# Optimization experiments

Measured on AMD Instinct MI355X. Metric: run time of the kernel, lower is better.

The kernel has to match this reference:

```python
import jax, jax.numpy as jnp
import numpy as np

B, S, D_MODEL, H, OUT = 32, 64, 256, 256, 10
N_POS = 64  # n_max_seq + 1


def _coordinate_map():
    i = jnp.arange(N_POS, dtype=jnp.float32)
    r = jnp.sqrt(jnp.float32(N_POS))
    c0 = (i / r - 2.0) / 2.0
    c1 = (jnp.mod(i, r) - 2.0) / 2.0
    coord = jnp.stack([c0, c1], axis=-1)            # [N_POS, 2]
    return jnp.broadcast_to(coord[None], (B, N_POS, 2))


def setup_inputs() -> dict:
    key = jax.random.key(0)
    ks = jax.random.split(key, 13)
    d_in = (D_MODEL + 2) * 3
    w = lambda k, i, o: jax.random.normal(k, (i, o), jnp.float32) * 0.02
    b = lambda k, o: jax.random.normal(k, (o,), jnp.float32) * 0.02
    return {
        'sentences': jax.random.normal(ks[0], (B, S, D_MODEL), jnp.float32),
        'coord': _coordinate_map(),
        'g_w1': w(ks[1], d_in, H), 'g_b1': b(ks[2], H),
        'g_w2': w(ks[3], H, H),    'g_b2': b(ks[4], H),
        'g_w3': w(ks[5], H, H),    'g_b3': b(ks[6], H),
        'f_w1': w(ks[7], H, H),    'f_b1': b(ks[8], H),
        'f_w2': w(ks[9], H, H),    'f_b2': b(ks[10], H),
        'f_w3': w(ks[11], H, OUT), 'f_b3': b(ks[12], OUT),
    }


def reference(sentences, coord, g_w1, g_b1, g_w2, g_b2, g_w3, g_b3,
              f_w1, f_b1, f_w2, f_b2, f_w3, f_b3):
    b, s, d = sentences.shape
    x = jnp.concatenate([sentences, coord[:b, :s, :]], axis=-1)   # [B,S,D+2]
    oi = jnp.broadcast_to(x[:, None, :, :], (b, s, s, d + 2))     # object_i[b,i,j]=x[b,j]
    oj = jnp.broadcast_to(x[:, :, None, :], (b, s, s, d + 2))     # object_j[b,i,j]=x[b,i]
    pairs = jnp.concatenate([oi, oj, oi * oj], axis=-1)           # [B,S,S,3*(D+2)]
    h = jax.nn.relu(jnp.einsum('bijk,kh->bijh', pairs, g_w1) + g_b1)
    h = jax.nn.relu(h @ g_w2 + g_b2)
    h = jax.nn.relu(h @ g_w3 + g_b3)
    rel = h.reshape(b, s * s, -1).sum(axis=1)                     # [B,H]
    y = jax.nn.relu(rel @ f_w1 + f_b1)
    y = jax.nn.relu(y @ f_w2 + f_b2)                              # Dropout: eval mode (identity)
    return y @ f_w3 + f_b3                                        # [B,OUT]
```

## Files before the change

### kernel.cpp

```cpp
#include <hip/hip_runtime.h>
#include <hip/hip_bf16.h>


typedef __attribute__((ext_vector_type(4))) float f32x4;
typedef __attribute__((ext_vector_type(16))) float f32x16;
typedef __attribute__((ext_vector_type(8))) short frag8;
typedef __attribute__((ext_vector_type(4))) unsigned u32x4;

__device__ __forceinline__ float bf2f(short s) {
  return __uint_as_float(((unsigned)(unsigned short)s) << 16);
}
__device__ __forceinline__ short f2bf(float f) {
  unsigned u = __float_as_uint(f);
  return (short)((u + 0x7fffu + ((u >> 16) & 1u)) >> 16);
}

__device__ __forceinline__ unsigned pk_bf16(float lo, float hi) {
#if __has_builtin(__builtin_amdgcn_cvt_pk_bf16_f32)
  return __builtin_bit_cast(unsigned, __builtin_amdgcn_cvt_pk_bf16_f32(lo, hi));
#else
  unsigned ul = __float_as_uint(lo), uh = __float_as_uint(hi);
  ul = (ul + 0x7fffu + ((ul >> 16) & 1u)) >> 16;
  uh = (uh + 0x7fffu + ((uh >> 16) & 1u)) & 0xffff0000u;
  return ul | uh;
#endif
}

__device__ __forceinline__ unsigned pk_mul_bf16(unsigned a, unsigned b) {
  float al = __uint_as_float(a << 16);
  float ah = __uint_as_float(a & 0xffff0000u);
  float bl = __uint_as_float(b << 16);
  float bh = __uint_as_float(b & 0xffff0000u);
  return pk_bf16(al * bl, ah * bh);
}

__device__ __forceinline__ frag8 pk_mul4(u32x4 a, u32x4 b) {
  u32x4 r;
#pragma unroll
  for (int t = 0; t < 4; t++) r[t] = pk_mul_bf16(a[t], b[t]);
  return __builtin_bit_cast(frag8, r);
}

#define KX 288

__global__ __launch_bounds__(256)
void prep(const float* __restrict__ sent, const float* __restrict__ coord,
          const float* __restrict__ g_w1, const float* __restrict__ g_w2,
          const float* __restrict__ g_w3,
          short* __restrict__ xb, short* __restrict__ Wab, short* __restrict__ Wc,
          short* __restrict__ W2t, short* __restrict__ W3t, float* __restrict__ rel) {
  __shared__ short tile[64 * 66];
  const int blk = blockIdx.x, t = threadIdx.x;

  if (blk < 288) {
    long idx0 = ((long)blk * 256 + t) * 8;
#pragma unroll
    for (int e = 0; e < 8; e++) {
      long idx = idx0 + e;
      int row = (int)(idx / KX), k = (int)(idx - (long)row * KX);
      float v = 0.f;
      if (k < 256)      v = sent[(size_t)row * 256 + k];
      else if (k < 258) v = coord[row * 2 + (k - 256)];
      xb[idx] = f2bf(v);
    }
    return;
  }

  const int nc = t & 63, r4 = t >> 6;
  if (blk < 328) {
    int tt = blk - 288, kt = tt >> 3, nt = tt & 7;
    int k0 = kt * 64, n0 = nt * 64;
    for (int p = 0; p < 16; p++) {
      int kl = p * 4 + r4, k = k0 + kl, n = n0 + nc;
      float v = 0.f;
      if (k < 258) {
        int row = (n < 256) ? k : 258 + k;
        int col = (n < 256) ? n : n - 256;
        v = g_w1[(size_t)row * 256 + col];
      }
      tile[kl * 66 + nc] = f2bf(v);
    }
    __syncthreads();
    for (int p = 0; p < 16; p++) {
      int nl = p * 4 + r4;
      if (k0 + nc < KX) Wab[(size_t)(n0 + nl) * KX + k0 + nc] = tile[nc * 66 + nl];
    }
    return;
  }
  if (blk < 348) {
    int tt = blk - 328, kt = tt >> 2, nt = tt & 3;
    int k0 = kt * 64, n0 = nt * 64;
    for (int p = 0; p < 16; p++) {
      int kl = p * 4 + r4, k = k0 + kl;
      float v = (k < 258) ? g_w1[(size_t)(516 + k) * 256 + n0 + nc] : 0.f;
      tile[kl * 66 + nc] = f2bf(v);
    }
    __syncthreads();
    for (int p = 0; p < 16; p++) {
      int nl = p * 4 + r4;
      if (k0 + nc < KX) Wc[(size_t)(n0 + nl) * KX + k0 + nc] = tile[nc * 66 + nl];
    }
    return;
  }
  if (blk < 380) {
    int tt = blk - 348;
    const float* W = (tt < 16) ? g_w2 : g_w3;
    short* Wt = (tt < 16) ? W2t : W3t;
    tt &= 15;
    int k0 = (tt >> 2) * 64, n0 = (tt & 3) * 64;
    for (int p = 0; p < 16; p++) {
      int kl = p * 4 + r4;
      tile[kl * 66 + nc] = f2bf(W[(size_t)(k0 + kl) * 256 + n0 + nc]);
    }
    __syncthreads();
    for (int p = 0; p < 16; p++) {
      int nl = p * 4 + r4;
      Wt[(size_t)(n0 + nl) * 256 + k0 + nc] = tile[nc * 66 + nl];
    }
    return;
  }
  {
    int bb = blk - 380;
    ((f32x4*)rel)[bb * 256 + t] = (f32x4){0.f, 0.f, 0.f, 0.f};
  }
}


__global__ __launch_bounds__(64)
void uv_gemm(const short* __restrict__ xb, const short* __restrict__ Wab,
             const float* __restrict__ g_b1, float* __restrict__ uv) {
  const int m0 = blockIdx.x * 64;
  const int n0 = blockIdx.y * 64;
  const int lane = threadIdx.x;
  const int q = lane >> 4, l16 = lane & 15;

  f32x4 acc[4][4];
#pragma unroll
  for (int mt = 0; mt < 4; mt++)
#pragma unroll
    for (int nt = 0; nt < 4; nt++) acc[mt][nt] = (f32x4){0.f, 0.f, 0.f, 0.f};

  for (int k0 = 0; k0 < KX; k0 += 32) {
    frag8 a[4], bb[4];
#pragma unroll
    for (int mt = 0; mt < 4; mt++)
      a[mt] = *(const frag8*)(xb + (size_t)(m0 + mt * 16 + l16) * KX + k0 + q * 8);
#pragma unroll
    for (int nt = 0; nt < 4; nt++)
      bb[nt] = *(const frag8*)(Wab + (size_t)(n0 + nt * 16 + l16) * KX + k0 + q * 8);
#pragma unroll
    for (int mt = 0; mt < 4; mt++)
#pragma unroll
      for (int nt = 0; nt < 4; nt++)
        acc[mt][nt] = __builtin_amdgcn_mfma_f32_16x16x32_bf16(a[mt], bb[nt], acc[mt][nt], 0, 0, 0);
  }
#pragma unroll
  for (int nt = 0; nt < 4; nt++) {
    int col = n0 + nt * 16 + l16;
    float bias = (col >= 256) ? g_b1[col - 256] : 0.f;
#pragma unroll
    for (int mt = 0; mt < 4; mt++) {
      int m = m0 + mt * 16 + q * 4;
#pragma unroll
      for (int r = 0; r < 4; r++)
        uv[(size_t)(m + r) * 512 + col] = acc[mt][nt][r] + bias;
    }
  }
}


#define LDS_SHORTS 32768

__global__ __launch_bounds__(256, 2)
void relnet_main(const short* __restrict__ xb, const short* __restrict__ Wc,
                 const short* __restrict__ W2t, const short* __restrict__ W3t,
                 const float* __restrict__ uv, const float* __restrict__ g_b2,
                 const float* __restrict__ g_b3, float* __restrict__ rel) {
  __shared__ short lds[LDS_SHORTS];

  const int tid = threadIdx.x;
  const int bi = blockIdx.x;
  const int b = bi >> 5, ip = bi & 31;
  const int i0 = ip * 2;
  const int lane = tid & 63, wave = tid >> 6;
  const int l32 = lane & 31, half = lane >> 5;
  const int n0 = wave * 64;
  const int rowbase = b * 64;

  f32x16 acc[4][2];
#pragma unroll
  for (int mt = 0; mt < 4; mt++)
#pragma unroll
    for (int nt = 0; nt < 2; nt++)
#pragma unroll
      for (int r = 0; r < 16; r++) acc[mt][nt][r] = 0.f;

  {
    const short* xjl = xb + (size_t)(rowbase + l32) * KX;
    const short* xjh = xb + (size_t)(rowbase + 32 + l32) * KX;
    const short* xi0p = xb + (size_t)(rowbase + i0) * KX;
    const short* xi1p = xb + (size_t)(rowbase + i0 + 1) * KX;
    const short* wc0 = Wc + (size_t)(n0 + l32) * KX;
    const short* wc1 = Wc + (size_t)(n0 + 32 + l32) * KX;

    u32x4 jl0, jh0, ia0, ib0, jl1, jh1, ia1, ib1;
    frag8 b0[2], b1[2];
    {
      int k = half * 8;
      jl0 = *(const u32x4*)(xjl + k);
      jh0 = *(const u32x4*)(xjh + k);
      ia0 = *(const u32x4*)(xi0p + k);
      ib0 = *(const u32x4*)(xi1p + k);
      b0[0] = *(const frag8*)(wc0 + k);
      b0[1] = *(const frag8*)(wc1 + k);
    }
#pragma unroll
    for (int ks = 0; ks < 18; ks++) {
      if (ks < 17) {
        int k = (ks + 1) * 16 + half * 8;
        jl1 = *(const u32x4*)(xjl + k);
        jh1 = *(const u32x4*)(xjh + k);
        ia1 = *(const u32x4*)(xi0p + k);
        ib1 = *(const u32x4*)(xi1p + k);
        b1[0] = *(const frag8*)(wc0 + k);
        b1[1] = *(const frag8*)(wc1 + k);
      }
      frag8 a[4];
      a[0] = pk_mul4(jl0, ia0);
      a[1] = pk_mul4(jh0, ia0);
      a[2] = pk_mul4(jl0, ib0);
      a[3] = pk_mul4(jh0, ib0);
#pragma unroll
      for (int mt = 0; mt < 4; mt++)
#pragma unroll
        for (int nt = 0; nt < 2; nt++)
          acc[mt][nt] = __builtin_amdgcn_mfma_f32_32x32x16_bf16(a[mt], b0[nt], acc[mt][nt], 0, 0, 0);
      jl0 = jl1; jh0 = jh1; ia0 = ia1; ib0 = ib1;
      b0[0] = b1[0]; b0[1] = b1[1];
    }
  }

  {
    const float* ub = uv + (size_t)rowbase * 512;
    const float* v0p = uv + (size_t)(rowbase + i0) * 512 + 256;
    const float* v1p = uv + (size_t)(rowbase + i0 + 1) * 512 + 256;
#pragma unroll
    for (int nt = 0; nt < 2; nt++) {
      int col = n0 + nt * 32 + l32;
      int cb = (n0 + nt * 32) >> 3;
      float vv0 = v0p[col], vv1 = v1p[col];
#pragma unroll
      for (int mt = 0; mt < 4; mt++) {
        float vv = (mt < 2) ? vv0 : vv1;
#pragma unroll
        for (int r = 0; r < 16; r += 2) {
          int rb0 = (r & 3) + 8 * (r >> 2) + 4 * half;
          int jm0 = (mt & 1) * 32 + rb0;
          float x0 = fmaxf(acc[mt][nt][r]     + ub[(size_t)jm0 * 512 + col] + vv, 0.f);
          float x1 = fmaxf(acc[mt][nt][r + 1] + ub[(size_t)(jm0 + 1) * 512 + col] + vv, 0.f);
          unsigned pk = pk_bf16(x0, x1);
          int m0r = mt * 32 + rb0;
          int sw0 = (r & 3) + 4 * half;
          lds[m0r * 256 + (((cb + (l32 >> 3)) ^ sw0) << 3) + (l32 & 7)] = (short)(pk & 0xffffu);
          lds[(m0r + 1) * 256 + (((cb + (l32 >> 3)) ^ (sw0 + 1)) << 3) + (l32 & 7)] = (short)(pk >> 16);
        }
#pragma unroll
        for (int r = 0; r < 16; r++) acc[mt][nt][r] = 0.f;
      }
    }
  }
  __syncthreads();

  {
    const int swr = l32 & 7;
    frag8 a0[4], b0[2], a1[4], b1[2];
#pragma unroll
    for (int mt = 0; mt < 4; mt++)
      a0[mt] = *(const frag8*)(&lds[(mt * 32 + l32) * 256 + ((half ^ swr) << 3)]);
#pragma unroll
    for (int nt = 0; nt < 2; nt++)
      b0[nt] = *(const frag8*)(W2t + (size_t)(n0 + nt * 32 + l32) * 256 + half * 8);
#pragma unroll
    for (int ks = 0; ks < 16; ks++) {
      if (ks < 15) {
        int c1 = ((2 * (ks + 1) + half) ^ swr) << 3;
        int k1 = (ks + 1) * 16 + half * 8;
#pragma unroll
        for (int mt = 0; mt < 4; mt++)
          a1[mt] = *(const frag8*)(&lds[(mt * 32 + l32) * 256 + c1]);
#pragma unroll
        for (int nt = 0; nt < 2; nt++)
          b1[nt] = *(const frag8*)(W2t + (size_t)(n0 + nt * 32 + l32) * 256 + k1);
      }
#pragma unroll
      for (int mt = 0; mt < 4; mt++)
#pragma unroll
        for (int nt = 0; nt < 2; nt++)
          acc[mt][nt] = __builtin_amdgcn_mfma_f32_32x32x16_bf16(a0[mt], b0[nt], acc[mt][nt], 0, 0, 0);
#pragma unroll
      for (int mt = 0; mt < 4; mt++) a0[mt] = a1[mt];
#pragma unroll
      for (int nt = 0; nt < 2; nt++) b0[nt] = b1[nt];
    }
  }
  __syncthreads();
#pragma unroll
  for (int nt = 0; nt < 2; nt++) {
    int col = n0 + nt * 32 + l32;
    int cb = (n0 + nt * 32) >> 3;
    float b2 = g_b2[col];
#pragma unroll
    for (int mt = 0; mt < 4; mt++) {
#pragma unroll
      for (int r = 0; r < 16; r += 2) {
        int rb0 = (r & 3) + 8 * (r >> 2) + 4 * half;
        float x0 = fmaxf(acc[mt][nt][r] + b2, 0.f);
        float x1 = fmaxf(acc[mt][nt][r + 1] + b2, 0.f);
        unsigned pk = pk_bf16(x0, x1);
        int m0r = mt * 32 + rb0;
        int sw0 = (r & 3) + 4 * half;
        lds[m0r * 256 + (((cb + (l32 >> 3)) ^ sw0) << 3) + (l32 & 7)] = (short)(pk & 0xffffu);
        lds[(m0r + 1) * 256 + (((cb + (l32 >> 3)) ^ (sw0 + 1)) << 3) + (l32 & 7)] = (short)(pk >> 16);
      }
#pragma unroll
      for (int r = 0; r < 16; r++) acc[mt][nt][r] = 0.f;
    }
  }
  __syncthreads();

  {
    const int swr = l32 & 7;
    frag8 a0[4], b0[2], a1[4], b1[2];
#pragma unroll
    for (int mt = 0; mt < 4; mt++)
      a0[mt] = *(const frag8*)(&lds[(mt * 32 + l32) * 256 + ((half ^ swr) << 3)]);
#pragma unroll
    for (int nt = 0; nt < 2; nt++)
      b0[nt] = *(const frag8*)(W3t + (size_t)(n0 + nt * 32 + l32) * 256 + half * 8);
#pragma unroll
    for (int ks = 0; ks < 16; ks++) {
      if (ks < 15) {
        int c1 = ((2 * (ks + 1) + half) ^ swr) << 3;
        int k1 = (ks + 1) * 16 + half * 8;
#pragma unroll
        for (int mt = 0; mt < 4; mt++)
          a1[mt] = *(const frag8*)(&lds[(mt * 32 + l32) * 256 + c1]);
#pragma unroll
        for (int nt = 0; nt < 2; nt++)
          b1[nt] = *(const frag8*)(W3t + (size_t)(n0 + nt * 32 + l32) * 256 + k1);
      }
#pragma unroll
      for (int mt = 0; mt < 4; mt++)
#pragma unroll
        for (int nt = 0; nt < 2; nt++)
          acc[mt][nt] = __builtin_amdgcn_mfma_f32_32x32x16_bf16(a0[mt], b0[nt], acc[mt][nt], 0, 0, 0);
#pragma unroll
      for (int mt = 0; mt < 4; mt++) a0[mt] = a1[mt];
#pragma unroll
      for (int nt = 0; nt < 2; nt++) b0[nt] = b1[nt];
    }
  }
#pragma unroll
  for (int nt = 0; nt < 2; nt++) {
    int col = n0 + nt * 32 + l32;
    float b3 = g_b3[col];
    float s = 0.f;
#pragma unroll
    for (int mt = 0; mt < 4; mt++)
#pragma unroll
      for (int r = 0; r < 16; r++)
        s += fmaxf(acc[mt][nt][r] + b3, 0.f);
    s += __shfl_xor(s, 32, 64);
    if (half == 0) atomicAdd(&rel[b * 256 + col], s);
  }
}

__global__ __launch_bounds__(256)
void fnet(const float* __restrict__ rel, const float* __restrict__ f_w1,
          const float* __restrict__ f_b1, const float* __restrict__ f_w2,
          const float* __restrict__ f_b2, const float* __restrict__ f_w3,
          const float* __restrict__ f_b3, float* __restrict__ out) {
  int b = blockIdx.x, t = threadIdx.x;
  __shared__ float y0[256], y1[256], y2[256];
  y0[t] = rel[b * 256 + t];
  __syncthreads();
  float s = f_b1[t];
#pragma unroll 8
  for (int k = 0; k < 256; k++) s += y0[k] * f_w1[k * 256 + t];
  y1[t] = fmaxf(s, 0.f);
  __syncthreads();
  s = f_b2[t];
#pragma unroll 8
  for (int k = 0; k < 256; k++) s += y1[k] * f_w2[k * 256 + t];
  y2[t] = fmaxf(s, 0.f);
  __syncthreads();
  if (t < 10) {
    float s2 = f_b3[t];
#pragma unroll 8
    for (int k = 0; k < 256; k++) s2 += y2[k] * f_w3[k * 10 + t];
    out[b * 10 + t] = s2;
  }
}

extern "C" void kernel_launch(void* const* d_in, const int* in_sizes, int n_in,
                              void* d_out, int out_size, void* d_ws, size_t ws_size,
                              hipStream_t stream) {
  const float* sent  = (const float*)d_in[0];
  const float* coord = (const float*)d_in[1];
  const float* g_w1  = (const float*)d_in[2];
  const float* g_b1  = (const float*)d_in[3];
  const float* g_w2  = (const float*)d_in[4];
  const float* g_b2  = (const float*)d_in[5];
  const float* g_w3  = (const float*)d_in[6];
  const float* g_b3  = (const float*)d_in[7];
  const float* f_w1  = (const float*)d_in[8];
  const float* f_b1  = (const float*)d_in[9];
  const float* f_w2  = (const float*)d_in[10];
  const float* f_b2  = (const float*)d_in[11];
  const float* f_w3  = (const float*)d_in[12];
  const float* f_b3  = (const float*)d_in[13];
  float* out = (float*)d_out;

  char* ws = (char*)d_ws;
  size_t off = 0;
  auto alloc = [&](size_t bytes) {
    char* p = ws + off;
    off += (bytes + 255) & ~(size_t)255;
    return p;
  };
  short* xb  = (short*)alloc((size_t)2048 * KX * 2);
  short* Wab = (short*)alloc((size_t)512 * KX * 2);
  short* Wc  = (short*)alloc((size_t)256 * KX * 2);
  short* W2t = (short*)alloc((size_t)256 * 256 * 2);
  short* W3t = (short*)alloc((size_t)256 * 256 * 2);
  float* uv  = (float*)alloc((size_t)2048 * 512 * 4);
  float* rel = (float*)alloc((size_t)32 * 256 * 4);

  prep<<<388, 256, 0, stream>>>(sent, coord, g_w1, g_w2, g_w3, xb, Wab, Wc, W2t, W3t, rel);
  uv_gemm<<<dim3(32, 8), 64, 0, stream>>>(xb, Wab, g_b1, uv);
  relnet_main<<<1024, 256, 0, stream>>>(xb, Wc, W2t, W3t, uv, g_b2, g_b3, rel);
  fnet<<<32, 256, 0, stream>>>(rel, f_w1, f_b1, f_w2, f_b2, f_w3, f_b3, out);
}
```

Baseline: 195.2 us.

## Stage pair products in LDS, transpose u buffer, double-buffer weight fragments

```diff
diff --git a/kernel.cpp b/kernel.cpp
--- a/kernel.cpp
+++ b/kernel.cpp
@@ -42,6 +42,7 @@
 }
 
 #define KX 288
+#define KS 272
 
 __global__ __launch_bounds__(256)
 void prep(const float* __restrict__ sent, const float* __restrict__ coord,
@@ -128,7 +129,8 @@
 
 __global__ __launch_bounds__(64)
 void uv_gemm(const short* __restrict__ xb, const short* __restrict__ Wab,
-             const float* __restrict__ g_b1, float* __restrict__ uv) {
+             const float* __restrict__ g_b1, float* __restrict__ uT,
+             float* __restrict__ vbuf) {
   const int m0 = blockIdx.x * 64;
   const int n0 = blockIdx.y * 64;
   const int lane = threadIdx.x;
@@ -154,28 +156,40 @@
       for (int nt = 0; nt < 4; nt++)
         acc[mt][nt] = __builtin_amdgcn_mfma_f32_16x16x32_bf16(a[mt], bb[nt], acc[mt][nt], 0, 0, 0);
   }
-#pragma unroll
-  for (int nt = 0; nt < 4; nt++) {
-    int col = n0 + nt * 16 + l16;
-    float bias = (col >= 256) ? g_b1[col - 256] : 0.f;
-#pragma unroll
-    for (int mt = 0; mt < 4; mt++) {
-      int m = m0 + mt * 16 + q * 4;
-#pragma unroll
-      for (int r = 0; r < 4; r++)
-        uv[(size_t)(m + r) * 512 + col] = acc[mt][nt][r] + bias;
-    }
-  }
-}
-
-
-#define LDS_SHORTS 32768
+  if (n0 < 256) {
+#pragma unroll
+    for (int nt = 0; nt < 4; nt++) {
+      int col = n0 + nt * 16 + l16;
+#pragma unroll
+      for (int mt = 0; mt < 4; mt++)
+        *(f32x4*)(uT + ((size_t)blockIdx.x * 256 + col) * 64 + mt * 16 + q * 4) = acc[mt][nt];
+    }
+  } else {
+#pragma unroll
+    for (int nt = 0; nt < 4; nt++) {
+      int c = n0 - 256 + nt * 16 + l16;
+      float bias = g_b1[c];
+#pragma unroll
+      for (int mt = 0; mt < 4; mt++) {
+        int m = m0 + mt * 16 + q * 4;
+#pragma unroll
+        for (int r = 0; r < 4; r++)
+          vbuf[(size_t)(m + r) * 256 + c] = acc[mt][nt][r] + bias;
+      }
+    }
+  }
+}
+
+
+#define ASH 280
+#define LDS_SHORTS (128 * ASH)
 
 __global__ __launch_bounds__(256, 2)
 void relnet_main(const short* __restrict__ xb, const short* __restrict__ Wc,
                  const short* __restrict__ W2t, const short* __restrict__ W3t,
-                 const float* __restrict__ uv, const float* __restrict__ g_b2,
-                 const float* __restrict__ g_b3, float* __restrict__ rel) {
+                 const float* __restrict__ uT, const float* __restrict__ vbuf,
+                 const float* __restrict__ g_b2, const float* __restrict__ g_b3,
+                 float* __restrict__ rel) {
   __shared__ short lds[LDS_SHORTS];
 
   const int tid = threadIdx.x;
@@ -186,6 +200,7 @@
   const int l32 = lane & 31, half = lane >> 5;
   const int n0 = wave * 64;
   const int rowbase = b * 64;
+  const int swr = l32 & 7;
 
   f32x16 acc[4][2];
 #pragma unroll
@@ -195,60 +210,52 @@
 #pragma unroll
       for (int r = 0; r < 16; r++) acc[mt][nt][r] = 0.f;
 
+#pragma unroll
+  for (int it = 0; it < 17; it++) {
+    int idx = tid + it * 256;
+    int j = idx / 34, c = idx - j * 34;
+    int k = c * 8;
+    u32x4 aj = *(const u32x4*)(xb + (size_t)(rowbase + (j & 63)) * KX + k);
+    u32x4 ai = *(const u32x4*)(xb + (size_t)(rowbase + i0 + (j >> 6)) * KX + k);
+    *(frag8*)(&lds[j * ASH + k]) = pk_mul4(aj, ai);
+  }
+
+  const short* wc0 = Wc + (size_t)(n0 + l32) * KX + half * 8;
+  const short* wc1 = Wc + (size_t)(n0 + 32 + l32) * KX + half * 8;
+  frag8 bp[2][2];
+  bp[0][0] = *(const frag8*)(wc0);
+  bp[0][1] = *(const frag8*)(wc1);
+  bp[1][0] = *(const frag8*)(wc0 + 16);
+  bp[1][1] = *(const frag8*)(wc1 + 16);
+  __syncthreads();
+
+#pragma unroll
+  for (int ks = 0; ks < 17; ks++) {
+    frag8 bc0 = bp[ks & 1][0], bc1 = bp[ks & 1][1];
+    if (ks + 2 < 17) {
+      bp[ks & 1][0] = *(const frag8*)(wc0 + (ks + 2) * 16);
+      bp[ks & 1][1] = *(const frag8*)(wc1 + (ks + 2) * 16);
+    }
+    frag8 a[4];
+#pragma unroll
+    for (int mt = 0; mt < 4; mt++)
+      a[mt] = *(const frag8*)(&lds[(mt * 32 + l32) * ASH + ks * 16 + half * 8]);
+#pragma unroll
+    for (int mt = 0; mt < 4; mt++) {
+      acc[mt][0] = __builtin_amdgcn_mfma_f32_32x32x16_bf16(a[mt], bc0, acc[mt][0], 0, 0, 0);
+      acc[mt][1] = __builtin_amdgcn_mfma_f32_32x32x16_bf16(a[mt], bc1, acc[mt][1], 0, 0, 0);
+    }
+  }
+  __syncthreads();
+
   {
-    const short* xjl = xb + (size_t)(rowbase + l32) * KX;
-    const short* xjh = xb + (size_t)(rowbase + 32 + l32) * KX;
-    const short* xi0p = xb + (size_t)(rowbase + i0) * KX;
-    const short* xi1p = xb + (size_t)(rowbase + i0 + 1) * KX;
-    const short* wc0 = Wc + (size_t)(n0 + l32) * KX;
-    const short* wc1 = Wc + (size_t)(n0 + 32 + l32) * KX;
-
-    u32x4 jl0, jh0, ia0, ib0, jl1, jh1, ia1, ib1;
-    frag8 b0[2], b1[2];
-    {
-      int k = half * 8;
-      jl0 = *(const u32x4*)(xjl + k);
-      jh0 = *(const u32x4*)(xjh + k);
-      ia0 = *(const u32x4*)(xi0p + k);
-      ib0 = *(const u32x4*)(xi1p + k);
-      b0[0] = *(const frag8*)(wc0 + k);
-      b0[1] = *(const frag8*)(wc1 + k);
-    }
-#pragma unroll
-    for (int ks = 0; ks < 18; ks++) {
-      if (ks < 17) {
-        int k = (ks + 1) * 16 + half * 8;
-        jl1 = *(const u32x4*)(xjl + k);
-        jh1 = *(const u32x4*)(xjh + k);
-        ia1 = *(const u32x4*)(xi0p + k);
-        ib1 = *(const u32x4*)(xi1p + k);
-        b1[0] = *(const frag8*)(wc0 + k);
-        b1[1] = *(const frag8*)(wc1 + k);
-      }
-      frag8 a[4];
-      a[0] = pk_mul4(jl0, ia0);
-      a[1] = pk_mul4(jh0, ia0);
-      a[2] = pk_mul4(jl0, ib0);
-      a[3] = pk_mul4(jh0, ib0);
-#pragma unroll
-      for (int mt = 0; mt < 4; mt++)
-#pragma unroll
-        for (int nt = 0; nt < 2; nt++)
-          acc[mt][nt] = __builtin_amdgcn_mfma_f32_32x32x16_bf16(a[mt], b0[nt], acc[mt][nt], 0, 0, 0);
-      jl0 = jl1; jh0 = jh1; ia0 = ia1; ib0 = ib1;
-      b0[0] = b1[0]; b0[1] = b1[1];
-    }
-  }
-
-  {
-    const float* ub = uv + (size_t)rowbase * 512;
-    const float* v0p = uv + (size_t)(rowbase + i0) * 512 + 256;
-    const float* v1p = uv + (size_t)(rowbase + i0 + 1) * 512 + 256;
 #pragma unroll
     for (int nt = 0; nt < 2; nt++) {
       int col = n0 + nt * 32 + l32;
       int cb = (n0 + nt * 32) >> 3;
-      float vv0 = v0p[col], vv1 = v1p[col];
+      const float* ubp = uT + ((size_t)b * 256 + col) * 64;
+      float vv0 = vbuf[(size_t)(rowbase + i0) * 256 + col];
+      float vv1 = vbuf[(size_t)(rowbase + i0 + 1) * 256 + col];
 #pragma unroll
       for (int mt = 0; mt < 4; mt++) {
         float vv = (mt < 2) ? vv0 : vv1;
@@ -256,8 +263,9 @@
         for (int r = 0; r < 16; r += 2) {
           int rb0 = (r & 3) + 8 * (r >> 2) + 4 * half;
           int jm0 = (mt & 1) * 32 + rb0;
-          float x0 = fmaxf(acc[mt][nt][r]     + ub[(size_t)jm0 * 512 + col] + vv, 0.f);
-          float x1 = fmaxf(acc[mt][nt][r + 1] + ub[(size_t)(jm0 + 1) * 512 + col] + vv, 0.f);
+          float2 uu = *(const float2*)(ubp + jm0);
+          float x0 = fmaxf(acc[mt][nt][r]     + uu.x + vv, 0.f);
+          float x1 = fmaxf(acc[mt][nt][r + 1] + uu.y + vv, 0.f);
           unsigned pk = pk_bf16(x0, x1);
           int m0r = mt * 32 + rb0;
           int sw0 = (r & 3) + 4 * half;
@@ -269,41 +277,33 @@
       }
     }
   }
-  __syncthreads();
-
-  {
-    const int swr = l32 & 7;
-    frag8 a0[4], b0[2], a1[4], b1[2];
-#pragma unroll
-    for (int mt = 0; mt < 4; mt++)
-      a0[mt] = *(const frag8*)(&lds[(mt * 32 + l32) * 256 + ((half ^ swr) << 3)]);
-#pragma unroll
-    for (int nt = 0; nt < 2; nt++)
-      b0[nt] = *(const frag8*)(W2t + (size_t)(n0 + nt * 32 + l32) * 256 + half * 8);
-#pragma unroll
-    for (int ks = 0; ks < 16; ks++) {
-      if (ks < 15) {
-        int c1 = ((2 * (ks + 1) + half) ^ swr) << 3;
-        int k1 = (ks + 1) * 16 + half * 8;
-#pragma unroll
-        for (int mt = 0; mt < 4; mt++)
-          a1[mt] = *(const frag8*)(&lds[(mt * 32 + l32) * 256 + c1]);
-#pragma unroll
-        for (int nt = 0; nt < 2; nt++)
-          b1[nt] = *(const frag8*)(W2t + (size_t)(n0 + nt * 32 + l32) * 256 + k1);
-      }
-#pragma unroll
-      for (int mt = 0; mt < 4; mt++)
-#pragma unroll
-        for (int nt = 0; nt < 2; nt++)
-          acc[mt][nt] = __builtin_amdgcn_mfma_f32_32x32x16_bf16(a0[mt], b0[nt], acc[mt][nt], 0, 0, 0);
-#pragma unroll
-      for (int mt = 0; mt < 4; mt++) a0[mt] = a1[mt];
-#pragma unroll
-      for (int nt = 0; nt < 2; nt++) b0[nt] = b1[nt];
-    }
-  }
-  __syncthreads();
+  const short* w20 = W2t + (size_t)(n0 + l32) * 256 + half * 8;
+  const short* w21 = W2t + (size_t)(n0 + 32 + l32) * 256 + half * 8;
+  bp[0][0] = *(const frag8*)(w20);
+  bp[0][1] = *(const frag8*)(w21);
+  bp[1][0] = *(const frag8*)(w20 + 16);
+  bp[1][1] = *(const frag8*)(w21 + 16);
+  __syncthreads();
+
+#pragma unroll
+  for (int ks = 0; ks < 16; ks++) {
+    frag8 bc0 = bp[ks & 1][0], bc1 = bp[ks & 1][1];
+    if (ks + 2 < 16) {
+      bp[ks & 1][0] = *(const frag8*)(w20 + (ks + 2) * 16);
+      bp[ks & 1][1] = *(const frag8*)(w21 + (ks + 2) * 16);
+    }
+    frag8 a[4];
+#pragma unroll
+    for (int mt = 0; mt < 4; mt++)
+      a[mt] = *(const frag8*)(&lds[(mt * 32 + l32) * 256 + (((2 * ks + half) ^ swr) << 3)]);
+#pragma unroll
+    for (int mt = 0; mt < 4; mt++) {
+      acc[mt][0] = __builtin_amdgcn_mfma_f32_32x32x16_bf16(a[mt], bc0, acc[mt][0], 0, 0, 0);
+      acc[mt][1] = __builtin_amdgcn_mfma_f32_32x32x16_bf16(a[mt], bc1, acc[mt][1], 0, 0, 0);
+    }
+  }
+  __syncthreads();
+
 #pragma unroll
   for (int nt = 0; nt < 2; nt++) {
     int col = n0 + nt * 32 + l32;
@@ -326,38 +326,29 @@
       for (int r = 0; r < 16; r++) acc[mt][nt][r] = 0.f;
     }
   }
-  __syncthreads();
-
-  {
-    const int swr = l32 & 7;
-    frag8 a0[4], b0[2], a1[4], b1[2];
-#pragma unroll
-    for (int mt = 0; mt < 4; mt++)
-      a0[mt] = *(const frag8*)(&lds[(mt * 32 + l32) * 256 + ((half ^ swr) << 3)]);
-#pragma unroll
-    for (int nt = 0; nt < 2; nt++)
-      b0[nt] = *(const frag8*)(W3t + (size_t)(n0 + nt * 32 + l32) * 256 + half * 8);
-#pragma unroll
-    for (int ks = 0; ks < 16; ks++) {
-      if (ks < 15) {
-        int c1 = ((2 * (ks + 1) + half) ^ swr) << 3;
-        int k1 = (ks + 1) * 16 + half * 8;
-#pragma unroll
-        for (int mt = 0; mt < 4; mt++)
-          a1[mt] = *(const frag8*)(&lds[(mt * 32 + l32) * 256 + c1]);
-#pragma unroll
-        for (int nt = 0; nt < 2; nt++)
-          b1[nt] = *(const frag8*)(W3t + (size_t)(n0 + nt * 32 + l32) * 256 + k1);
-      }
-#pragma unroll
-      for (int mt = 0; mt < 4; mt++)
-#pragma unroll
-        for (int nt = 0; nt < 2; nt++)
-          acc[mt][nt] = __builtin_amdgcn_mfma_f32_32x32x16_bf16(a0[mt], b0[nt], acc[mt][nt], 0, 0, 0);
-#pragma unroll
-      for (int mt = 0; mt < 4; mt++) a0[mt] = a1[mt];
-#pragma unroll
-      for (int nt = 0; nt < 2; nt++) b0[nt] = b1[nt];
+  const short* w30 = W3t + (size_t)(n0 + l32) * 256 + half * 8;
+  const short* w31 = W3t + (size_t)(n0 + 32 + l32) * 256 + half * 8;
+  bp[0][0] = *(const frag8*)(w30);
+  bp[0][1] = *(const frag8*)(w31);
+  bp[1][0] = *(const frag8*)(w30 + 16);
+  bp[1][1] = *(const frag8*)(w31 + 16);
+  __syncthreads();
+
+#pragma unroll
+  for (int ks = 0; ks < 16; ks++) {
+    frag8 bc0 = bp[ks & 1][0], bc1 = bp[ks & 1][1];
+    if (ks + 2 < 16) {
+      bp[ks & 1][0] = *(const frag8*)(w30 + (ks + 2) * 16);
+      bp[ks & 1][1] = *(const frag8*)(w31 + (ks + 2) * 16);
+    }
+    frag8 a[4];
+#pragma unroll
+    for (int mt = 0; mt < 4; mt++)
+      a[mt] = *(const frag8*)(&lds[(mt * 32 + l32) * 256 + (((2 * ks + half) ^ swr) << 3)]);
+#pragma unroll
+    for (int mt = 0; mt < 4; mt++) {
+      acc[mt][0] = __builtin_amdgcn_mfma_f32_32x32x16_bf16(a[mt], bc0, acc[mt][0], 0, 0, 0);
+      acc[mt][1] = __builtin_amdgcn_mfma_f32_32x32x16_bf16(a[mt], bc1, acc[mt][1], 0, 0, 0);
     }
   }
 #pragma unroll
@@ -428,16 +419,17 @@
     off += (bytes + 255) & ~(size_t)255;
     return p;
   };
-  short* xb  = (short*)alloc((size_t)2048 * KX * 2);
-  short* Wab = (short*)alloc((size_t)512 * KX * 2);
-  short* Wc  = (short*)alloc((size_t)256 * KX * 2);
-  short* W2t = (short*)alloc((size_t)256 * 256 * 2);
-  short* W3t = (short*)alloc((size_t)256 * 256 * 2);
-  float* uv  = (float*)alloc((size_t)2048 * 512 * 4);
-  float* rel = (float*)alloc((size_t)32 * 256 * 4);
+  short* xb   = (short*)alloc((size_t)2048 * KX * 2);
+  short* Wab  = (short*)alloc((size_t)512 * KX * 2);
+  short* Wc   = (short*)alloc((size_t)256 * KX * 2);
+  short* W2t  = (short*)alloc((size_t)256 * 256 * 2);
+  short* W3t  = (short*)alloc((size_t)256 * 256 * 2);
+  float* uT   = (float*)alloc((size_t)32 * 256 * 64 * 4);
+  float* vbuf = (float*)alloc((size_t)2048 * 256 * 4);
+  float* rel  = (float*)alloc((size_t)32 * 256 * 4);
 
   prep<<<388, 256, 0, stream>>>(sent, coord, g_w1, g_w2, g_w3, xb, Wab, Wc, W2t, W3t, rel);
-  uv_gemm<<<dim3(32, 8), 64, 0, stream>>>(xb, Wab, g_b1, uv);
-  relnet_main<<<1024, 256, 0, stream>>>(xb, Wc, W2t, W3t, uv, g_b2, g_b3, rel);
+  uv_gemm<<<dim3(32, 8), 64, 0, stream>>>(xb, Wab, g_b1, uT, vbuf);
+  relnet_main<<<1024, 256, 0, stream>>>(xb, Wc, W2t, W3t, uT, vbuf, g_b2, g_b3, rel);
   fnet<<<32, 256, 0, stream>>>(rel, f_w1, f_b1, f_w2, f_b2, f_w3, f_b3, out);
 }
```

Measured after the change: 217.5 us. 1.11x slower.

## Stage elementwise-product A tile in LDS once instead of per-wave recompute

Applied to the files above, without the earlier changes.

```diff
diff --git a/kernel.cpp b/kernel.cpp
--- a/kernel.cpp
+++ b/kernel.cpp
@@ -169,7 +169,9 @@
 }
 
 
-#define LDS_SHORTS 32768
+#define ASH 152
+#define A2OFF (128 * ASH)
+#define LDS_SHORTS (2 * 128 * ASH)
 
 __global__ __launch_bounds__(256, 2)
 void relnet_main(const short* __restrict__ xb, const short* __restrict__ Wc,
@@ -186,6 +188,7 @@
   const int l32 = lane & 31, half = lane >> 5;
   const int n0 = wave * 64;
   const int rowbase = b * 64;
+  const int swr = l32 & 7;
 
   f32x16 acc[4][2];
 #pragma unroll
@@ -195,50 +198,90 @@
 #pragma unroll
       for (int r = 0; r < 16; r++) acc[mt][nt][r] = 0.f;
 
-  {
-    const short* xjl = xb + (size_t)(rowbase + l32) * KX;
-    const short* xjh = xb + (size_t)(rowbase + 32 + l32) * KX;
-    const short* xi0p = xb + (size_t)(rowbase + i0) * KX;
-    const short* xi1p = xb + (size_t)(rowbase + i0 + 1) * KX;
-    const short* wc0 = Wc + (size_t)(n0 + l32) * KX;
-    const short* wc1 = Wc + (size_t)(n0 + 32 + l32) * KX;
-
-    u32x4 jl0, jh0, ia0, ib0, jl1, jh1, ia1, ib1;
-    frag8 b0[2], b1[2];
-    {
-      int k = half * 8;
-      jl0 = *(const u32x4*)(xjl + k);
-      jh0 = *(const u32x4*)(xjh + k);
-      ia0 = *(const u32x4*)(xi0p + k);
-      ib0 = *(const u32x4*)(xi1p + k);
-      b0[0] = *(const frag8*)(wc0 + k);
-      b0[1] = *(const frag8*)(wc1 + k);
-    }
-#pragma unroll
-    for (int ks = 0; ks < 18; ks++) {
-      if (ks < 17) {
-        int k = (ks + 1) * 16 + half * 8;
-        jl1 = *(const u32x4*)(xjl + k);
-        jh1 = *(const u32x4*)(xjh + k);
-        ia1 = *(const u32x4*)(xi0p + k);
-        ib1 = *(const u32x4*)(xi1p + k);
-        b1[0] = *(const frag8*)(wc0 + k);
-        b1[1] = *(const frag8*)(wc1 + k);
-      }
-      frag8 a[4];
-      a[0] = pk_mul4(jl0, ia0);
-      a[1] = pk_mul4(jh0, ia0);
-      a[2] = pk_mul4(jl0, ib0);
-      a[3] = pk_mul4(jh0, ib0);
+#pragma unroll
+  for (int it = 0; it < 9; it++) {
+    int idx = tid + it * 256;
+    int j = idx / 18, c = idx - j * 18;
+    int k = c * 8;
+    u32x4 aj = *(const u32x4*)(xb + (size_t)(rowbase + (j & 63)) * KX + k);
+    u32x4 ai = *(const u32x4*)(xb + (size_t)(rowbase + i0 + (j >> 6)) * KX + k);
+    *(frag8*)(&lds[j * ASH + k]) = pk_mul4(aj, ai);
+  }
+  __syncthreads();
+
+  {
+    frag8 a0[4], b0[2], a1[4], b1[2];
+#pragma unroll
+    for (int mt = 0; mt < 4; mt++)
+      a0[mt] = *(const frag8*)(&lds[(mt * 32 + l32) * ASH + half * 8]);
+#pragma unroll
+    for (int nt = 0; nt < 2; nt++)
+      b0[nt] = *(const frag8*)(Wc + (size_t)(n0 + nt * 32 + l32) * KX + half * 8);
+#pragma unroll
+    for (int ks = 0; ks < 9; ks++) {
+      if (ks < 8) {
+        int k1 = (ks + 1) * 16 + half * 8;
+#pragma unroll
+        for (int mt = 0; mt < 4; mt++)
+          a1[mt] = *(const frag8*)(&lds[(mt * 32 + l32) * ASH + k1]);
+#pragma unroll
+        for (int nt = 0; nt < 2; nt++)
+          b1[nt] = *(const frag8*)(Wc + (size_t)(n0 + nt * 32 + l32) * KX + k1);
+      }
 #pragma unroll
       for (int mt = 0; mt < 4; mt++)
 #pragma unroll
         for (int nt = 0; nt < 2; nt++)
-          acc[mt][nt] = __builtin_amdgcn_mfma_f32_32x32x16_bf16(a[mt], b0[nt], acc[mt][nt], 0, 0, 0);
-      jl0 = jl1; jh0 = jh1; ia0 = ia1; ib0 = ib1;
-      b0[0] = b1[0]; b0[1] = b1[1];
-    }
-  }
+          acc[mt][nt] = __builtin_amdgcn_mfma_f32_32x32x16_bf16(a0[mt], b0[nt], acc[mt][nt], 0, 0, 0);
+#pragma unroll
+      for (int mt = 0; mt < 4; mt++) a0[mt] = a1[mt];
+#pragma unroll
+      for (int nt = 0; nt < 2; nt++) b0[nt] = b1[nt];
+    }
+  }
+
+#pragma unroll
+  for (int it = 0; it < 8; it++) {
+    int idx = tid + it * 256;
+    int j = idx >> 4, c = idx & 15;
+    int k = 144 + c * 8;
+    u32x4 aj = *(const u32x4*)(xb + (size_t)(rowbase + (j & 63)) * KX + k);
+    u32x4 ai = *(const u32x4*)(xb + (size_t)(rowbase + i0 + (j >> 6)) * KX + k);
+    *(frag8*)(&lds[A2OFF + j * ASH + c * 8]) = pk_mul4(aj, ai);
+  }
+  __syncthreads();
+
+  {
+    frag8 a0[4], b0[2], a1[4], b1[2];
+#pragma unroll
+    for (int mt = 0; mt < 4; mt++)
+      a0[mt] = *(const frag8*)(&lds[A2OFF + (mt * 32 + l32) * ASH + half * 8]);
+#pragma unroll
+    for (int nt = 0; nt < 2; nt++)
+      b0[nt] = *(const frag8*)(Wc + (size_t)(n0 + nt * 32 + l32) * KX + 144 + half * 8);
+#pragma unroll
+    for (int ks = 0; ks < 8; ks++) {
+      if (ks < 7) {
+        int k1 = (ks + 1) * 16 + half * 8;
+#pragma unroll
+        for (int mt = 0; mt < 4; mt++)
+          a1[mt] = *(const frag8*)(&lds[A2OFF + (mt * 32 + l32) * ASH + k1]);
+#pragma unroll
+        for (int nt = 0; nt < 2; nt++)
+          b1[nt] = *(const frag8*)(Wc + (size_t)(n0 + nt * 32 + l32) * KX + 144 + k1);
+      }
+#pragma unroll
+      for (int mt = 0; mt < 4; mt++)
+#pragma unroll
+        for (int nt = 0; nt < 2; nt++)
+          acc[mt][nt] = __builtin_amdgcn_mfma_f32_32x32x16_bf16(a0[mt], b0[nt], acc[mt][nt], 0, 0, 0);
+#pragma unroll
+      for (int mt = 0; mt < 4; mt++) a0[mt] = a1[mt];
+#pragma unroll
+      for (int nt = 0; nt < 2; nt++) b0[nt] = b1[nt];
+    }
+  }
+  __syncthreads();
 
   {
     const float* ub = uv + (size_t)rowbase * 512;
@@ -272,7 +315,6 @@
   __syncthreads();
 
   {
-    const int swr = l32 & 7;
     frag8 a0[4], b0[2], a1[4], b1[2];
 #pragma unroll
     for (int mt = 0; mt < 4; mt++)
@@ -304,6 +346,7 @@
     }
   }
   __syncthreads();
+
 #pragma unroll
   for (int nt = 0; nt < 2; nt++) {
     int col = n0 + nt * 32 + l32;
@@ -329,7 +372,6 @@
   __syncthreads();
 
   {
-    const int swr = l32 & 7;
     frag8 a0[4], b0[2], a1[4], b1[2];
 #pragma unroll
     for (int mt = 0; mt < 4; mt++)
```

Result: faster. 183.2 us (-6.2%).

## Use 8 waves per block and stage pairwise product tiles in LDS

Applied to the files above, without the earlier changes.

```diff
diff --git a/kernel.cpp b/kernel.cpp
--- a/kernel.cpp
+++ b/kernel.cpp
@@ -169,9 +169,11 @@
 }
 
 
-#define LDS_SHORTS 32768
-
-__global__ __launch_bounds__(256, 2)
+#define ASH 152
+#define A2OFF (128 * ASH)
+#define LDS_SHORTS (2 * 128 * ASH)
+
+__global__ __launch_bounds__(512, 4)
 void relnet_main(const short* __restrict__ xb, const short* __restrict__ Wc,
                  const short* __restrict__ W2t, const short* __restrict__ W3t,
                  const float* __restrict__ uv, const float* __restrict__ g_b2,
@@ -184,138 +186,68 @@
   const int i0 = ip * 2;
   const int lane = tid & 63, wave = tid >> 6;
   const int l32 = lane & 31, half = lane >> 5;
-  const int n0 = wave * 64;
+  const int n0 = wave * 32;
   const int rowbase = b * 64;
-
-  f32x16 acc[4][2];
+  const int swr = l32 & 7;
+  const int col = n0 + l32;
+  const int cb = n0 >> 3;
+
+  f32x16 acc[4];
 #pragma unroll
   for (int mt = 0; mt < 4; mt++)
 #pragma unroll
-    for (int nt = 0; nt < 2; nt++)
-#pragma unroll
-      for (int r = 0; r < 16; r++) acc[mt][nt][r] = 0.f;
-
-  {
-    const short* xjl = xb + (size_t)(rowbase + l32) * KX;
-    const short* xjh = xb + (size_t)(rowbase + 32 + l32) * KX;
-    const short* xi0p = xb + (size_t)(rowbase + i0) * KX;
-    const short* xi1p = xb + (size_t)(rowbase + i0 + 1) * KX;
-    const short* wc0 = Wc + (size_t)(n0 + l32) * KX;
-    const short* wc1 = Wc + (size_t)(n0 + 32 + l32) * KX;
-
-    u32x4 jl0, jh0, ia0, ib0, jl1, jh1, ia1, ib1;
-    frag8 b0[2], b1[2];
-    {
-      int k = half * 8;
-      jl0 = *(const u32x4*)(xjl + k);
-      jh0 = *(const u32x4*)(xjh + k);
-      ia0 = *(const u32x4*)(xi0p + k);
-      ib0 = *(const u32x4*)(xi1p + k);
-      b0[0] = *(const frag8*)(wc0 + k);
-      b0[1] = *(const frag8*)(wc1 + k);
-    }
-#pragma unroll
-    for (int ks = 0; ks < 18; ks++) {
-      if (ks < 17) {
-        int k = (ks + 1) * 16 + half * 8;
-        jl1 = *(const u32x4*)(xjl + k);
-        jh1 = *(const u32x4*)(xjh + k);
-        ia1 = *(const u32x4*)(xi0p + k);
-        ib1 = *(const u32x4*)(xi1p + k);
-        b1[0] = *(const frag8*)(wc0 + k);
-        b1[1] = *(const frag8*)(wc1 + k);
+    for (int r = 0; r < 16; r++) acc[mt][r] = 0.f;
+
+#pragma unroll
+  for (int it = 0; it < 9; it++) {
+    int idx = tid + it * 512;
+    if (idx < 4352) {
+      int j = idx / 34, c = idx - j * 34;
+      int k = c * 8;
+      u32x4 aj = *(const u32x4*)(xb + (size_t)(rowbase + (j & 63)) * KX + k);
+      u32x4 ai = *(const u32x4*)(xb + (size_t)(rowbase + i0 + (j >> 6)) * KX + k);
+      frag8 pr = pk_mul4(aj, ai);
+      if (c < 18) *(frag8*)(&lds[j * ASH + k]) = pr;
+      else        *(frag8*)(&lds[A2OFF + j * ASH + (k - 144)]) = pr;
+    }
+  }
+  __syncthreads();
+
+  {
+    const short* wc = Wc + (size_t)(n0 + l32) * KX + half * 8;
+    frag8 b0 = *(const frag8*)(wc);
+#pragma unroll
+    for (int ks = 0; ks < 17; ks++) {
+      frag8 b1;
+      if (ks < 16) b1 = *(const frag8*)(wc + (ks + 1) * 16);
+      frag8 a[4];
+#pragma unroll
+      for (int mt = 0; mt < 4; mt++) {
+        int base = (ks < 9) ? ((mt * 32 + l32) * ASH + ks * 16 + half * 8)
+                            : (A2OFF + (mt * 32 + l32) * ASH + (ks - 9) * 16 + half * 8);
+        a[mt] = *(const frag8*)(&lds[base]);
       }
-      frag8 a[4];
-      a[0] = pk_mul4(jl0, ia0);
-      a[1] = pk_mul4(jh0, ia0);
-      a[2] = pk_mul4(jl0, ib0);
-      a[3] = pk_mul4(jh0, ib0);
-#pragma unroll
-      for (int mt = 0; mt < 4; mt++)
-#pragma unroll
-        for (int nt = 0; nt < 2; nt++)
-          acc[mt][nt] = __builtin_amdgcn_mfma_f32_32x32x16_bf16(a[mt], b0[nt], acc[mt][nt], 0, 0, 0);
-      jl0 = jl1; jh0 = jh1; ia0 = ia1; ib0 = ib1;
-      b0[0] = b1[0]; b0[1] = b1[1];
-    }
-  }
+#pragma unroll
+      for (int mt = 0; mt < 4; mt++)
+        acc[mt] = __builtin_amdgcn_mfma_f32_32x32x16_bf16(a[mt], b0, acc[mt], 0, 0, 0);
+      b0 = b1;
+    }
+  }
+  __syncthreads();
 
   {
     const float* ub = uv + (size_t)rowbase * 512;
-    const float* v0p = uv + (size_t)(rowbase + i0) * 512 + 256;
-    const float* v1p = uv + (size_t)(rowbase + i0 + 1) * 512 + 256;
-#pragma unroll
-    for (int nt = 0; nt < 2; nt++) {
-      int col = n0 + nt * 32 + l32;
-      int cb = (n0 + nt * 32) >> 3;
-      float vv0 = v0p[col], vv1 = v1p[col];
-#pragma unroll
-      for (int mt = 0; mt < 4; mt++) {
-        float vv = (mt < 2) ? vv0 : vv1;
-#pragma unroll
-        for (int r = 0; r < 16; r += 2) {
-          int rb0 = (r & 3) + 8 * (r >> 2) + 4 * half;
-          int jm0 = (mt & 1) * 32 + rb0;
-          float x0 = fmaxf(acc[mt][nt][r]     + ub[(size_t)jm0 * 512 + col] + vv, 0.f);
-          float x1 = fmaxf(acc[mt][nt][r + 1] + ub[(size_t)(jm0 + 1) * 512 + col] + vv, 0.f);
-          unsigned pk = pk_bf16(x0, x1);
-          int m0r = mt * 32 + rb0;
-          int sw0 = (r & 3) + 4 * half;
-          lds[m0r * 256 + (((cb + (l32 >> 3)) ^ sw0) << 3) + (l32 & 7)] = (short)(pk & 0xffffu);
-          lds[(m0r + 1) * 256 + (((cb + (l32 >> 3)) ^ (sw0 + 1)) << 3) + (l32 & 7)] = (short)(pk >> 16);
-        }
-#pragma unroll
-        for (int r = 0; r < 16; r++) acc[mt][nt][r] = 0.f;
-      }
-    }
-  }
-  __syncthreads();
-
-  {
-    const int swr = l32 & 7;
-    frag8 a0[4], b0[2], a1[4], b1[2];
-#pragma unroll
-    for (int mt = 0; mt < 4; mt++)
-      a0[mt] = *(const frag8*)(&lds[(mt * 32 + l32) * 256 + ((half ^ swr) << 3)]);
-#pragma unroll
-    for (int nt = 0; nt < 2; nt++)
-      b0[nt] = *(const frag8*)(W2t + (size_t)(n0 + nt * 32 + l32) * 256 + half * 8);
-#pragma unroll
-    for (int ks = 0; ks < 16; ks++) {
-      if (ks < 15) {
-        int c1 = ((2 * (ks + 1) + half) ^ swr) << 3;
-        int k1 = (ks + 1) * 16 + half * 8;
-#pragma unroll
-        for (int mt = 0; mt < 4; mt++)
-          a1[mt] = *(const frag8*)(&lds[(mt * 32 + l32) * 256 + c1]);
-#pragma unroll
-        for (int nt = 0; nt < 2; nt++)
-          b1[nt] = *(const frag8*)(W2t + (size_t)(n0 + nt * 32 + l32) * 256 + k1);
-      }
-#pragma unroll
-      for (int mt = 0; mt < 4; mt++)
-#pragma unroll
-        for (int nt = 0; nt < 2; nt++)
-          acc[mt][nt] = __builtin_amdgcn_mfma_f32_32x32x16_bf16(a0[mt], b0[nt], acc[mt][nt], 0, 0, 0);
-#pragma unroll
-      for (int mt = 0; mt < 4; mt++) a0[mt] = a1[mt];
-#pragma unroll
-      for (int nt = 0; nt < 2; nt++) b0[nt] = b1[nt];
-    }
-  }
-  __syncthreads();
-#pragma unroll
-  for (int nt = 0; nt < 2; nt++) {
-    int col = n0 + nt * 32 + l32;
-    int cb = (n0 + nt * 32) >> 3;
-    float b2 = g_b2[col];
+    float vv0 = uv[(size_t)(rowbase + i0) * 512 + 256 + col];
+    float vv1 = uv[(size_t)(rowbase + i0 + 1) * 512 + 256 + col];
 #pragma unroll
     for (int mt = 0; mt < 4; mt++) {
+      float vv = (mt < 2) ? vv0 : vv1;
 #pragma unroll
       for (int r = 0; r < 16; r += 2) {
         int rb0 = (r & 3) + 8 * (r >> 2) + 4 * half;
-        float x0 = fmaxf(acc[mt][nt][r] + b2, 0.f);
-        float x1 = fmaxf(acc[mt][nt][r + 1] + b2, 0.f);
+        int jm0 = (mt & 1) * 32 + rb0;
+        float x0 = fmaxf(acc[mt][r]     + ub[(size_t)jm0 * 512 + col] + vv, 0.f);
+        float x1 = fmaxf(acc[mt][r + 1] + ub[(size_t)(jm0 + 1) * 512 + col] + vv, 0.f);
         unsigned pk = pk_bf16(x0, x1);
         int m0r = mt * 32 + rb0;
         int sw0 = (r & 3) + 4 * half;
@@ -323,53 +255,76 @@
         lds[(m0r + 1) * 256 + (((cb + (l32 >> 3)) ^ (sw0 + 1)) << 3) + (l32 & 7)] = (short)(pk >> 16);
       }
 #pragma unroll
-      for (int r = 0; r < 16; r++) acc[mt][nt][r] = 0.f;
-    }
-  }
-  __syncthreads();
-
-  {
-    const int swr = l32 & 7;
-    frag8 a0[4], b0[2], a1[4], b1[2];
-#pragma unroll
-    for (int mt = 0; mt < 4; mt++)
-      a0[mt] = *(const frag8*)(&lds[(mt * 32 + l32) * 256 + ((half ^ swr) << 3)]);
-#pragma unroll
-    for (int nt = 0; nt < 2; nt++)
-      b0[nt] = *(const frag8*)(W3t + (size_t)(n0 + nt * 32 + l32) * 256 + half * 8);
+      for (int r = 0; r < 16; r++) acc[mt][r] = 0.f;
+    }
+  }
+  __syncthreads();
+
+  {
+    const short* w2 = W2t + (size_t)(n0 + l32) * 256 + half * 8;
+    frag8 b0 = *(const frag8*)(w2);
 #pragma unroll
     for (int ks = 0; ks < 16; ks++) {
-      if (ks < 15) {
-        int c1 = ((2 * (ks + 1) + half) ^ swr) << 3;
-        int k1 = (ks + 1) * 16 + half * 8;
-#pragma unroll
-        for (int mt = 0; mt < 4; mt++)
-          a1[mt] = *(const frag8*)(&lds[(mt * 32 + l32) * 256 + c1]);
-#pragma unroll
-        for (int nt = 0; nt < 2; nt++)
-          b1[nt] = *(const frag8*)(W3t + (size_t)(n0 + nt * 32 + l32) * 256 + k1);
+      frag8 b1;
+      if (ks < 15) b1 = *(const frag8*)(w2 + (ks + 1) * 16);
+      frag8 a[4];
+#pragma unroll
+      for (int mt = 0; mt < 4; mt++)
+        a[mt] = *(const frag8*)(&lds[(mt * 32 + l32) * 256 + (((2 * ks + half) ^ swr) << 3)]);
+#pragma unroll
+      for (int mt = 0; mt < 4; mt++)
+        acc[mt] = __builtin_amdgcn_mfma_f32_32x32x16_bf16(a[mt], b0, acc[mt], 0, 0, 0);
+      b0 = b1;
+    }
+  }
+  __syncthreads();
+
+  {
+    float b2 = g_b2[col];
+#pragma unroll
+    for (int mt = 0; mt < 4; mt++) {
+#pragma unroll
+      for (int r = 0; r < 16; r += 2) {
+        int rb0 = (r & 3) + 8 * (r >> 2) + 4 * half;
+        float x0 = fmaxf(acc[mt][r] + b2, 0.f);
+        float x1 = fmaxf(acc[mt][r + 1] + b2, 0.f);
+        unsigned pk = pk_bf16(x0, x1);
+        int m0r = mt * 32 + rb0;
+        int sw0 = (r & 3) + 4 * half;
+        lds[m0r * 256 + (((cb + (l32 >> 3)) ^ sw0) << 3) + (l32 & 7)] = (short)(pk & 0xffffu);
+        lds[(m0r + 1) * 256 + (((cb + (l32 >> 3)) ^ (sw0 + 1)) << 3) + (l32 & 7)] = (short)(pk >> 16);
       }
 #pragma unroll
-      for (int mt = 0; mt < 4; mt++)
-#pragma unroll
-        for (int nt = 0; nt < 2; nt++)
-          acc[mt][nt] = __builtin_amdgcn_mfma_f32_32x32x16_bf16(a0[mt], b0[nt], acc[mt][nt], 0, 0, 0);
-#pragma unroll
-      for (int mt = 0; mt < 4; mt++) a0[mt] = a1[mt];
-#pragma unroll
-      for (int nt = 0; nt < 2; nt++) b0[nt] = b1[nt];
-    }
-  }
-#pragma unroll
-  for (int nt = 0; nt < 2; nt++) {
-    int col = n0 + nt * 32 + l32;
+      for (int r = 0; r < 16; r++) acc[mt][r] = 0.f;
+    }
+  }
+  __syncthreads();
+
+  {
+    const short* w3 = W3t + (size_t)(n0 + l32) * 256 + half * 8;
+    frag8 b0 = *(const frag8*)(w3);
+#pragma unroll
+    for (int ks = 0; ks < 16; ks++) {
+      frag8 b1;
+      if (ks < 15) b1 = *(const frag8*)(w3 + (ks + 1) * 16);
+      frag8 a[4];
+#pragma unroll
+      for (int mt = 0; mt < 4; mt++)
+        a[mt] = *(const frag8*)(&lds[(mt * 32 + l32) * 256 + (((2 * ks + half) ^ swr) << 3)]);
+#pragma unroll
+      for (int mt = 0; mt < 4; mt++)
+        acc[mt] = __builtin_amdgcn_mfma_f32_32x32x16_bf16(a[mt], b0, acc[mt], 0, 0, 0);
+      b0 = b1;
+    }
+  }
+  {
     float b3 = g_b3[col];
     float s = 0.f;
 #pragma unroll
     for (int mt = 0; mt < 4; mt++)
 #pragma unroll
       for (int r = 0; r < 16; r++)
-        s += fmaxf(acc[mt][nt][r] + b3, 0.f);
+        s += fmaxf(acc[mt][r] + b3, 0.f);
     s += __shfl_xor(s, 32, 64);
     if (half == 0) atomicAdd(&rel[b * 256 + col], s);
   }
@@ -438,6 +393,6 @@
 
   prep<<<388, 256, 0, stream>>>(sent, coord, g_w1, g_w2, g_w3, xb, Wab, Wc, W2t, W3t, rel);
   uv_gemm<<<dim3(32, 8), 64, 0, stream>>>(xb, Wab, g_b1, uv);
-  relnet_main<<<1024, 256, 0, stream>>>(xb, Wc, W2t, W3t, uv, g_b2, g_b3, rel);
+  relnet_main<<<1024, 512, 0, stream>>>(xb, Wc, W2t, W3t, uv, g_b2, g_b3, rel);
   fnet<<<32, 256, 0, stream>>>(rel, f_w1, f_b1, f_w2, f_b2, f_w3, f_b3, out);
 }
```

After: 198.8 us. About the same (+1.8%).
